# Optimization experiments

Measured on AMD Instinct MI355X. Metric: run time of the kernel, lower is better.

The kernel has to match this reference:

```python
import jax, jax.numpy as jnp
import numpy as np

B, T, C, H = 4, 2048, 1024, 16
HS = C // H  # head_size = 64
FF = 4 * C   # 4096
EPS = 1e-5


def _layernorm(x, g, b):
    mu = jnp.mean(x, axis=-1, keepdims=True)
    var = jnp.mean(jnp.square(x - mu), axis=-1, keepdims=True)
    return (x - mu) * jax.lax.rsqrt(var + EPS) * g + b


def setup_inputs() -> dict:
    key = jax.random.key(0)
    ks = jax.random.split(key, 12)
    s_in = 1.0 / np.sqrt(C)
    s_ff = 1.0 / np.sqrt(FF)
    return {
        "x": jax.random.normal(ks[0], (B, T, C), jnp.float32),
        # per-head projection weights stacked: [H, C, HS]
        "Wq": jax.random.normal(ks[1], (H, C, HS), jnp.float32) * s_in,
        "Wk": jax.random.normal(ks[2], (H, C, HS), jnp.float32) * s_in,
        "Wv": jax.random.normal(ks[3], (H, C, HS), jnp.float32) * s_in,
        "Wo": jax.random.normal(ks[4], (C, C), jnp.float32) * s_in,
        "bo": jnp.zeros((C,), jnp.float32),
        "g1": jnp.ones((C,), jnp.float32),
        "b1": jnp.zeros((C,), jnp.float32),
        "g2": jnp.ones((C,), jnp.float32),
        "b2": jnp.zeros((C,), jnp.float32),
        "W1": jax.random.normal(ks[5], (C, FF), jnp.float32) * s_in,
        "bf1": jnp.zeros((FF,), jnp.float32),
        "W2": jax.random.normal(ks[6], (FF, C), jnp.float32) * s_ff,
        "bf2": jnp.zeros((C,), jnp.float32),
    }


def reference(x, Wq, Wk, Wv, Wo, bo, g1, b1, g2, b2, W1, bf1, W2, bf2):
    # pre-norm
    h = _layernorm(x, g1, b1)                       # [B,T,C]
    q = jnp.einsum('btc,hcd->bhtd', h, Wq)          # [B,H,T,HS]
    k = jnp.einsum('btc,hcd->bhtd', h, Wk)
    v = jnp.einsum('btc,hcd->bhtd', h, Wv)
    w = jnp.einsum('bhtd,bhsd->bhts', q, k) * (HS ** -0.5)  # [B,H,T,S]
    mask = jnp.tril(jnp.ones((T, T), bool))          # causal tril
    w = jnp.where(mask[None, None], w, -jnp.inf)
    # NB: original code softmaxes over dim=1 of [B,T,T], i.e. the QUERY axis
    w = jax.nn.softmax(w, axis=-2)
    o = jnp.einsum('bhts,bhsd->bhtd', w, v)          # [B,H,T,HS]
    o = jnp.transpose(o, (0, 2, 1, 3)).reshape(B, T, C)  # concat heads
    x = x + o @ Wo + bo                              # residual 1 (dropout=0)
    f = _layernorm(x, g2, b2)
    ff = jax.nn.relu(f @ W1 + bf1) @ W2 + bf2        # FFN (dropout=0)
    return x + ff
```

## Files before the change

### kernel.cpp

```cpp
#include <hip/hip_runtime.h>


#define T_SEQ 2048
#define SCALE2 0.1803368801f

typedef __attribute__((ext_vector_type(8))) short short8;
typedef __attribute__((ext_vector_type(4))) float f32x4;

typedef __attribute__((address_space(1))) unsigned int g_u32;
typedef __attribute__((address_space(3))) unsigned int l_u32;

__device__ __forceinline__ unsigned short f2bf(float f) {
  union { float f; unsigned u; } x; x.f = f;
  unsigned r = (x.u + 0x7FFFu + ((x.u >> 16) & 1u)) >> 16;
  return (unsigned short)r;
}
__device__ __forceinline__ float bf2f(unsigned short u) {
  union { unsigned u; float f; } x; x.u = (unsigned)u << 16;
  return x.f;
}

__device__ __forceinline__ void g2lds16(const void* g, void* l) {
  __builtin_amdgcn_global_load_lds((g_u32*)g, (l_u32*)l, 16, 0, 0);
}

__device__ __forceinline__ int xcd_swz(int flat, int nwg) {
  if ((nwg & 7) != 0) return flat;
  return (flat & 7) * (nwg >> 3) + (flat >> 3);
}

template <int EPI, int BN>
__global__ __launch_bounds__(512, 2) void gemm256(
    const unsigned short* __restrict__ A, const unsigned short* __restrict__ Bt,
    int M, int N, int K,
    unsigned short* __restrict__ out16, float* __restrict__ outF,
    const float* __restrict__ bias, const float* __restrict__ resid) {
  constexpr int WN = BN / 4;
  constexpr int FN = WN / 16;
  extern __shared__ unsigned short lds[];
  unsigned short* ldsA = lds;
  unsigned short* ldsB = lds + 2 * 16384;
  const int tid = threadIdx.x, lane = tid & 63, wid = tid >> 6;
  const int wm = wid >> 2, wn = wid & 3;
  const int nx = gridDim.x;
  const int flat = blockIdx.y * nx + blockIdx.x;
  const int swz = xcd_swz(flat, nx * gridDim.y);
  const int mBase = (swz / nx) * 256, nBase = (swz % nx) * BN;

  f32x4 acc[8][FN];
#pragma unroll
  for (int i = 0; i < 8; ++i)
#pragma unroll
    for (int j = 0; j < FN; ++j)
#pragma unroll
      for (int e = 0; e < 4; ++e) acc[i][j][e] = 0.f;

  auto stage = [&](int buf, int kt) {
    const int k0 = kt << 6;
#pragma unroll
    for (int it = 0; it < 4; ++it) {
      int g = it * 512 + tid;
      int row = g >> 3, colL = g & 7;
      int col = colL ^ (row & 7);
      g2lds16(A + ((size_t)(mBase + row) * K + k0 + col * 8),
              &ldsA[buf * 16384 + (it * 512 + wid * 64) * 8]);
    }
#pragma unroll
    for (int it = 0; it < (BN * 8) / 512; ++it) {
      int g = it * 512 + tid;
      int row = g >> 3, colL = g & 7;
      int col = colL ^ (row & 7);
      g2lds16(Bt + ((size_t)(nBase + row) * K + k0 + col * 8),
              &ldsB[buf * (BN * 64) + (it * 512 + wid * 64) * 8]);
    }
  };

  const int nKT = K >> 6;
  stage(0, 0);
  __syncthreads();
  int cur = 0;
  for (int kt = 0; kt < nKT; ++kt) {
    if (kt + 1 < nKT) stage(cur ^ 1, kt + 1);

    short8 bf[FN][2];
#pragma unroll
    for (int fn = 0; fn < FN; ++fn)
#pragma unroll
      for (int ks = 0; ks < 2; ++ks) {
        int r = wn * WN + fn * 16 + (lane & 15);
        int c = (ks * 4 + (lane >> 4)) ^ (r & 7);
        bf[fn][ks] = *(const short8*)&ldsB[cur * (BN * 64) + r * 64 + c * 8];
      }
#pragma unroll
    for (int q = 0; q < 4; ++q) {
      short8 af[2][2];
#pragma unroll
      for (int mf = 0; mf < 2; ++mf)
#pragma unroll
        for (int ks = 0; ks < 2; ++ks) {
          int r = wm * 128 + q * 32 + mf * 16 + (lane & 15);
          int c = (ks * 4 + (lane >> 4)) ^ (r & 7);
          af[mf][ks] = *(const short8*)&ldsA[cur * 16384 + r * 64 + c * 8];
        }
      __builtin_amdgcn_s_setprio(1);
#pragma unroll
      for (int mf = 0; mf < 2; ++mf)
#pragma unroll
        for (int fn = 0; fn < FN; ++fn)
#pragma unroll
          for (int ks = 0; ks < 2; ++ks)
            acc[q * 2 + mf][fn] = __builtin_amdgcn_mfma_f32_16x16x32_bf16(
                af[mf][ks], bf[fn][ks], acc[q * 2 + mf][fn], 0, 0, 0);
      __builtin_amdgcn_s_setprio(0);
    }
    __syncthreads();
    cur ^= 1;
  }

#pragma unroll
  for (int am = 0; am < 8; ++am)
#pragma unroll
    for (int fn = 0; fn < FN; ++fn) {
      int col = nBase + wn * WN + fn * 16 + (lane & 15);
      int row0 = mBase + wm * 128 + am * 16 + ((lane >> 4) << 2);
      if (EPI == 0) {
#pragma unroll
        for (int r = 0; r < 4; ++r)
          out16[(size_t)(row0 + r) * N + col] = f2bf(acc[am][fn][r]);
      } else if (EPI == 1) {
        float bv = bias[col];
#pragma unroll
        for (int r = 0; r < 4; ++r) {
          size_t idx = (size_t)(row0 + r) * N + col;
          outF[idx] = acc[am][fn][r] + bv + resid[idx];
        }
      } else {
        float bv = bias[col];
#pragma unroll
        for (int r = 0; r < 4; ++r)
          out16[(size_t)(row0 + r) * N + col] =
              f2bf(fmaxf(acc[am][fn][r] + bv, 0.f));
      }
    }
}

__global__ __launch_bounds__(256) void ln_bf16(
    const float* __restrict__ x, const float* __restrict__ gw,
    const float* __restrict__ bw, unsigned short* __restrict__ out) {
  __shared__ float red[8];
  const int row = blockIdx.x, tid = threadIdx.x;
  const float4 v = ((const float4*)(x + (size_t)row * 1024))[tid];
  float s = v.x + v.y + v.z + v.w;
  float q = v.x * v.x + v.y * v.y + v.z * v.z + v.w * v.w;
#pragma unroll
  for (int off = 32; off >= 1; off >>= 1) {
    s += __shfl_down(s, off);
    q += __shfl_down(q, off);
  }
  const int lane = tid & 63, wid = tid >> 6;
  if (lane == 0) { red[wid] = s; red[4 + wid] = q; }
  __syncthreads();
  float S = red[0] + red[1] + red[2] + red[3];
  float Q = red[4] + red[5] + red[6] + red[7];
  float mu = S * (1.f / 1024.f);
  float var = Q * (1.f / 1024.f) - mu * mu;
  float rs = rsqrtf(var + 1e-5f);
  int c = tid * 4;
  ushort4 ov;
  ov.x = f2bf((v.x - mu) * rs * gw[c + 0] + bw[c + 0]);
  ov.y = f2bf((v.y - mu) * rs * gw[c + 1] + bw[c + 1]);
  ov.z = f2bf((v.z - mu) * rs * gw[c + 2] + bw[c + 2]);
  ov.w = f2bf((v.w - mu) * rs * gw[c + 3] + bw[c + 3]);
  *(ushort4*)&out[(size_t)row * 1024 + c] = ov;
}

__global__ __launch_bounds__(256) void pack_qkv(
    const float* __restrict__ Wq, const float* __restrict__ Wk,
    const float* __restrict__ Wv, unsigned short* __restrict__ out) {
  __shared__ float tile[64 * 65];
  const int tid = threadIdx.x;
  const float* W = (blockIdx.z == 0) ? Wq : (blockIdx.z == 1) ? Wk : Wv;
  const int h = blockIdx.y, r0 = blockIdx.x * 64;
#pragma unroll
  for (int it = 0; it < 4; ++it) {
    int e4 = it * 256 + tid;
    int r = e4 >> 4, c4 = e4 & 15;
    float4 v = *(const float4*)&W[((size_t)h * 1024 + r0 + r) * 64 + c4 * 4];
    tile[r * 65 + c4 * 4 + 0] = v.x;
    tile[r * 65 + c4 * 4 + 1] = v.y;
    tile[r * 65 + c4 * 4 + 2] = v.z;
    tile[r * 65 + c4 * 4 + 3] = v.w;
  }
  __syncthreads();
#pragma unroll
  for (int it = 0; it < 4; ++it) {
    int e4 = it * 256 + tid;
    int d = e4 >> 4, r4 = e4 & 15;
    ushort4 ov;
    ov.x = f2bf(tile[(r4 * 4 + 0) * 65 + d]);
    ov.y = f2bf(tile[(r4 * 4 + 1) * 65 + d]);
    ov.z = f2bf(tile[(r4 * 4 + 2) * 65 + d]);
    ov.w = f2bf(tile[(r4 * 4 + 3) * 65 + d]);
    *(ushort4*)&out[(size_t)(blockIdx.z * 1024 + h * 64 + d) * 1024 + r0 +
                    r4 * 4] = ov;
  }
}

__global__ __launch_bounds__(256) void transpose_cast(
    const float* __restrict__ in, unsigned short* __restrict__ out, int R,
    int C) {
  __shared__ float tile[64 * 65];
  const int tid = threadIdx.x;
  const int r0 = blockIdx.x * 64, c0 = blockIdx.y * 64;
#pragma unroll
  for (int it = 0; it < 4; ++it) {
    int e4 = it * 256 + tid;
    int r = e4 >> 4, c4 = e4 & 15;
    float4 v = *(const float4*)&in[(size_t)(r0 + r) * C + c0 + c4 * 4];
    tile[r * 65 + c4 * 4 + 0] = v.x;
    tile[r * 65 + c4 * 4 + 1] = v.y;
    tile[r * 65 + c4 * 4 + 2] = v.z;
    tile[r * 65 + c4 * 4 + 3] = v.w;
  }
  __syncthreads();
#pragma unroll
  for (int it = 0; it < 4; ++it) {
    int e4 = it * 256 + tid;
    int c = e4 >> 4, r4 = e4 & 15;
    ushort4 ov;
    ov.x = f2bf(tile[(r4 * 4 + 0) * 65 + c]);
    ov.y = f2bf(tile[(r4 * 4 + 1) * 65 + c]);
    ov.z = f2bf(tile[(r4 * 4 + 2) * 65 + c]);
    ov.w = f2bf(tile[(r4 * 4 + 3) * 65 + c]);
    *(ushort4*)&out[(size_t)(c0 + c) * R + r0 + r4 * 4] = ov;
  }
}

__global__ __launch_bounds__(256) void vtrans(
    const unsigned short* __restrict__ qkv, const float* __restrict__ linv,
    unsigned short* __restrict__ vT) {
  __shared__ unsigned short tile[64 * 66];
  const int tid = threadIdx.x;
  const int bh = blockIdx.y, b = bh >> 4, h = bh & 15;
  const int t0 = blockIdx.x * 64;
#pragma unroll
  for (int it = 0; it < 8; ++it) {
    int e2 = it * 256 + tid;
    int r = e2 >> 5, c2 = e2 & 31;
    unsigned v = *(const unsigned*)&qkv[(size_t)(b * T_SEQ + t0 + r) * 3072 +
                                        2048 + h * 64 + c2 * 2];
    float li = linv[(size_t)bh * T_SEQ + t0 + r];
    unsigned short lo = f2bf(bf2f((unsigned short)(v & 0xffff)) * li);
    unsigned short hi = f2bf(bf2f((unsigned short)(v >> 16)) * li);
    *(unsigned*)&tile[r * 66 + c2 * 2] = (unsigned)lo | ((unsigned)hi << 16);
  }
  __syncthreads();
#pragma unroll
  for (int it = 0; it < 8; ++it) {
    int e2 = it * 256 + tid;
    int d = e2 >> 5, t2 = e2 & 31;
    unsigned short a = tile[(t2 * 2) * 66 + d];
    unsigned short bb = tile[(t2 * 2 + 1) * 66 + d];
    unsigned pk = (unsigned)a | ((unsigned)bb << 16);
    *(unsigned*)&vT[(size_t)(bh * 64 + d) * T_SEQ + t0 + t2 * 2] = pk;
  }
}

__global__ __launch_bounds__(256) void attn_stats(
    const unsigned short* __restrict__ qkv, float* __restrict__ linvOut) {
  __shared__ unsigned short qt[2][64 * 64];
  const int tid = threadIdx.x, lane = tid & 63, w = tid >> 6;
  const int f = xcd_swz(blockIdx.y * 8 + blockIdx.x, 512);
  const int q = f & 7, bh = f >> 3;
  const int b = bh >> 4, h = bh & 15;
  const int sxA = q * 4 + w, sxB = 31 - sxA;
  const int sA = sxA * 64, sB = sxB * 64;
  const int it0 = (q <= 3) ? 4 * q : 28 - 4 * q;

  short8 kfA[4][2], kfB[4][2];
#pragma unroll
  for (int fn = 0; fn < 4; ++fn)
#pragma unroll
    for (int ks = 0; ks < 2; ++ks) {
      int d = 1024 + h * 64 + ks * 32 + ((lane >> 4) << 3);
      kfA[fn][ks] = *(const short8*)&qkv[(size_t)(b * T_SEQ + sA + fn * 16 +
                                                  (lane & 15)) * 3072 + d];
      kfB[fn][ks] = *(const short8*)&qkv[(size_t)(b * T_SEQ + sB + fn * 16 +
                                                  (lane & 15)) * 3072 + d];
    }
  float lA[4] = {0.f, 0.f, 0.f, 0.f}, lB[4] = {0.f, 0.f, 0.f, 0.f};

  auto stageQ = [&](int buf, int ti) {
    int t0 = ti * 64;
#pragma unroll
    for (int it = 0; it < 2; ++it) {
      int g = it * 256 + tid;
      int row = g >> 3;
      int col = (g & 7) ^ (row & 7);
      g2lds16(qkv + ((size_t)(b * T_SEQ + t0 + row) * 3072 + h * 64 + col * 8),
              &qt[buf][(it * 256 + w * 64) * 8]);
    }
  };

  auto accum = [&](const short8 (&af)[2], const short8 (&kf)[4][2],
                   float (&lacc)[4], int sBase, int t0, int mf, bool diag) {
    f32x4 sc[4];
#pragma unroll
    for (int fn = 0; fn < 4; ++fn)
#pragma unroll
      for (int e = 0; e < 4; ++e) sc[fn][e] = 0.f;
    __builtin_amdgcn_s_setprio(1);
#pragma unroll
    for (int fn = 0; fn < 4; ++fn)
#pragma unroll
      for (int ks = 0; ks < 2; ++ks)
        sc[fn] = __builtin_amdgcn_mfma_f32_16x16x32_bf16(af[ks], kf[fn][ks],
                                                         sc[fn], 0, 0, 0);
    __builtin_amdgcn_s_setprio(0);
    const int tRow = t0 + mf * 16 + ((lane >> 4) << 2);
    if (diag) {
#pragma unroll
      for (int fn = 0; fn < 4; ++fn) {
        int s = sBase + fn * 16 + (lane & 15);
#pragma unroll
        for (int r = 0; r < 4; ++r) {
          float e = exp2f(sc[fn][r] * SCALE2);
          lacc[fn] += (tRow + r >= s) ? e : 0.f;
        }
      }
    } else {
#pragma unroll
      for (int fn = 0; fn < 4; ++fn)
#pragma unroll
        for (int r = 0; r < 4; ++r) lacc[fn] += exp2f(sc[fn][r] * SCALE2);
    }
  };

  stageQ(0, it0);
  __syncthreads();
  int cur = 0;
  for (int ti = it0; ti < 32; ++ti) {
    if (ti + 1 < 32) stageQ(cur ^ 1, ti + 1);
    const bool doA = ti >= sxA, doB = ti >= sxB;
    if (doA | doB) {
      const int t0g = ti * 64;
#pragma unroll
      for (int mf = 0; mf < 4; ++mf) {
        short8 af[2];
#pragma unroll
        for (int ks = 0; ks < 2; ++ks) {
          int r = mf * 16 + (lane & 15);
          int c = (ks * 4 + (lane >> 4)) ^ (r & 7);
          af[ks] = *(const short8*)&qt[cur][r * 64 + c * 8];
        }
        if (doA) accum(af, kfA, lA, sA, t0g, mf, ti == sxA);
        if (doB) accum(af, kfB, lB, sB, t0g, mf, ti == sxB);
      }
    }
    __syncthreads();
    cur ^= 1;
  }
#pragma unroll
  for (int fn = 0; fn < 4; ++fn) {
    lA[fn] += __shfl_down(lA[fn], 32);
    lA[fn] += __shfl_down(lA[fn], 16);
    lB[fn] += __shfl_down(lB[fn], 32);
    lB[fn] += __shfl_down(lB[fn], 16);
  }
  if (lane < 16) {
#pragma unroll
    for (int fn = 0; fn < 4; ++fn) {
      linvOut[(size_t)bh * T_SEQ + sA + fn * 16 + lane] = 1.f / lA[fn];
      linvOut[(size_t)bh * T_SEQ + sB + fn * 16 + lane] = 1.f / lB[fn];
    }
  }
}

__global__ __launch_bounds__(256, 2) void attn_pv(
    const unsigned short* __restrict__ qkv, const unsigned short* __restrict__ vT,
    unsigned short* __restrict__ o) {
  __shared__ unsigned short kbuf[2][64 * 64];
  __shared__ unsigned short vbuf[2][64 * 64];
  __shared__ unsigned short pl[256 * 64];
  const int tid = threadIdx.x, lane = tid & 63, wid = tid >> 6;
  const int f = xcd_swz(blockIdx.y * 8 + blockIdx.x, 512);
  const int bx = f & 7, bh = f >> 3;
  const int b = bh >> 4, h = bh & 15;
  const int tA = bx * 128, tB = (15 - bx) * 128;
  const int nSTA = 2 * bx + 2, nSTB = 32 - 2 * bx;

  short8 qfA[2][2], qfB[2][2];
#pragma unroll
  for (int mf = 0; mf < 2; ++mf)
#pragma unroll
    for (int ks = 0; ks < 2; ++ks) {
      int d = h * 64 + ks * 32 + ((lane >> 4) << 3);
      int rloc = wid * 32 + mf * 16 + (lane & 15);
      qfA[mf][ks] =
          *(const short8*)&qkv[(size_t)(b * T_SEQ + tA + rloc) * 3072 + d];
      qfB[mf][ks] =
          *(const short8*)&qkv[(size_t)(b * T_SEQ + tB + rloc) * 3072 + d];
    }
  f32x4 oaccA[2][4], oaccB[2][4];
#pragma unroll
  for (int i = 0; i < 2; ++i)
#pragma unroll
    for (int j = 0; j < 4; ++j)
#pragma unroll
      for (int e = 0; e < 4; ++e) { oaccA[i][j][e] = 0.f; oaccB[i][j][e] = 0.f; }

  auto stage = [&](int buf, int st) {
#pragma unroll
    for (int it = 0; it < 2; ++it) {
      int g = it * 256 + tid;
      int row = g >> 3, colL = g & 7;
      int col = colL ^ (row & 7);
      g2lds16(qkv + ((size_t)(b * T_SEQ + st * 64 + row) * 3072 + 1024 +
                     h * 64 + col * 8),
              &kbuf[buf][(it * 256 + wid * 64) * 8]);
      g2lds16(vT + ((size_t)(bh * 64 + row) * T_SEQ + st * 64 + col * 8),
              &vbuf[buf][(it * 256 + wid * 64) * 8]);
    }
  };

  auto qkstore = [&](const short8 (&qf)[2][2], int rowBase, int tBase, int s0,
                     bool maskNeeded, int cur) {
    f32x4 sc[2][4];
#pragma unroll
    for (int i = 0; i < 2; ++i)
#pragma unroll
      for (int j = 0; j < 4; ++j)
#pragma unroll
        for (int e = 0; e < 4; ++e) sc[i][j][e] = 0.f;
    __builtin_amdgcn_s_setprio(1);
#pragma unroll
    for (int fn = 0; fn < 4; ++fn)
#pragma unroll
      for (int ks = 0; ks < 2; ++ks) {
        int r = fn * 16 + (lane & 15);
        int c = (ks * 4 + (lane >> 4)) ^ (r & 7);
        short8 kfr = *(const short8*)&kbuf[cur][r * 64 + c * 8];
        sc[0][fn] = __builtin_amdgcn_mfma_f32_16x16x32_bf16(qf[0][ks], kfr,
                                                            sc[0][fn], 0, 0, 0);
        sc[1][fn] = __builtin_amdgcn_mfma_f32_16x16x32_bf16(qf[1][ks], kfr,
                                                            sc[1][fn], 0, 0, 0);
      }
    __builtin_amdgcn_s_setprio(0);
#pragma unroll
    for (int fn = 0; fn < 4; ++fn) {
      int sg = s0 + fn * 16 + (lane & 15);
      int colb = (fn * 16 + (lane & 15)) * 2;
#pragma unroll
      for (int mf = 0; mf < 2; ++mf) {
        int rowB = rowBase + wid * 32 + mf * 16 + ((lane >> 4) << 2);
        int tRow = tBase + wid * 32 + mf * 16 + ((lane >> 4) << 2);
#pragma unroll
        for (int r = 0; r < 4; ++r) {
          float p = exp2f(sc[mf][fn][r] * SCALE2);
          if (maskNeeded) p = (tRow + r >= sg) ? p : 0.f;
          int row = rowB + r;
          int byteoff = row * 128 + (colb ^ ((row & 7) << 4));
          *(unsigned short*)((char*)pl + byteoff) = f2bf(p);
        }
      }
    }
  };

  stage(0, 0);
  int cur = 0;
  __syncthreads();

  for (int st = 0; st < nSTB; ++st) {
    const int s0 = st * 64;
    const bool doA = st < nSTA;

    if (doA) qkstore(qfA, 0, tA, s0, st >= nSTA - 2, cur);
    qkstore(qfB, 128, tB, s0, st >= nSTB - 2, cur);
    __syncthreads();

    if (st + 1 < nSTB) stage(cur ^ 1, st + 1);

    __builtin_amdgcn_s_setprio(1);
#pragma unroll
    for (int ks = 0; ks < 2; ++ks) {
      short8 paA[2], paB[2];
#pragma unroll
      for (int mf = 0; mf < 2; ++mf) {
        int rowa = wid * 32 + mf * 16 + (lane & 15);
        int kb = ks * 64 + ((lane >> 4) << 4);
        paB[mf] = *(const short8*)((const char*)pl + (128 + rowa) * 128 +
                                   (kb ^ ((rowa & 7) << 4)));
        if (doA)
          paA[mf] = *(const short8*)((const char*)pl + rowa * 128 +
                                     (kb ^ ((rowa & 7) << 4)));
      }
#pragma unroll
      for (int df = 0; df < 4; ++df) {
        int r = df * 16 + (lane & 15);
        int c = (ks * 4 + (lane >> 4)) ^ (r & 7);
        short8 vb = *(const short8*)&vbuf[cur][r * 64 + c * 8];
        oaccB[0][df] = __builtin_amdgcn_mfma_f32_16x16x32_bf16(paB[0], vb,
                                                               oaccB[0][df], 0, 0, 0);
        oaccB[1][df] = __builtin_amdgcn_mfma_f32_16x16x32_bf16(paB[1], vb,
                                                               oaccB[1][df], 0, 0, 0);
        if (doA) {
          oaccA[0][df] = __builtin_amdgcn_mfma_f32_16x16x32_bf16(paA[0], vb,
                                                                 oaccA[0][df], 0, 0, 0);
          oaccA[1][df] = __builtin_amdgcn_mfma_f32_16x16x32_bf16(paA[1], vb,
                                                                 oaccA[1][df], 0, 0, 0);
        }
      }
    }
    __builtin_amdgcn_s_setprio(0);
    __syncthreads();
    cur ^= 1;
  }
#pragma unroll
  for (int mf = 0; mf < 2; ++mf)
#pragma unroll
    for (int df = 0; df < 4; ++df) {
      int d = h * 64 + df * 16 + (lane & 15);
      int ra = tA + wid * 32 + mf * 16 + ((lane >> 4) << 2);
      int rb = tB + wid * 32 + mf * 16 + ((lane >> 4) << 2);
#pragma unroll
      for (int r = 0; r < 4; ++r) {
        o[(size_t)(b * T_SEQ + ra + r) * 1024 + d] = f2bf(oaccA[mf][df][r]);
        o[(size_t)(b * T_SEQ + rb + r) * 1024 + d] = f2bf(oaccB[mf][df][r]);
      }
    }
}

extern "C" void kernel_launch(void* const* d_in, const int* in_sizes, int n_in,
                              void* d_out, int out_size, void* d_ws,
                              size_t ws_size, hipStream_t stream) {
  const float* x = (const float*)d_in[0];
  const float* Wq = (const float*)d_in[1];
  const float* Wk = (const float*)d_in[2];
  const float* Wv = (const float*)d_in[3];
  const float* Wo = (const float*)d_in[4];
  const float* bo = (const float*)d_in[5];
  const float* g1 = (const float*)d_in[6];
  const float* b1 = (const float*)d_in[7];
  const float* g2 = (const float*)d_in[8];
  const float* b2 = (const float*)d_in[9];
  const float* W1 = (const float*)d_in[10];
  const float* bf1 = (const float*)d_in[11];
  const float* W2 = (const float*)d_in[12];
  const float* bf2 = (const float*)d_in[13];
  float* out = (float*)d_out;

  char* ws = (char*)d_ws;
  size_t off = 0;
  auto alloc = [&](size_t bytes) {
    char* p = ws + off;
    off += (bytes + 255) & ~(size_t)255;
    return p;
  };
  unsigned short* Wqkv = (unsigned short*)alloc(3072ull * 1024 * 2);
  unsigned short* WoT = (unsigned short*)alloc(1024ull * 1024 * 2);
  unsigned short* W1T = (unsigned short*)alloc(4096ull * 1024 * 2);
  unsigned short* W2T = (unsigned short*)alloc(1024ull * 4096 * 2);
  unsigned short* hbuf = (unsigned short*)alloc(8192ull * 1024 * 2);
  char* regionE = alloc(8192ull * 3072 * 2 + 64ull * 64 * 2048 * 2);
  unsigned short* qkv = (unsigned short*)regionE;
  unsigned short* vT = (unsigned short*)(regionE + 8192ull * 3072 * 2);
  unsigned short* act = (unsigned short*)regionE;
  float* lbuf = (float*)alloc(64ull * 2048 * 4);
  float* x1 = (float*)alloc(8192ull * 1024 * 4);
  unsigned short* fbuf = (unsigned short*)alloc(8192ull * 1024 * 2);
  unsigned short* obuf = hbuf;

  (void)in_sizes; (void)n_in; (void)out_size; (void)ws_size;

  const size_t LDS128 = (2 * 16384 + 2 * 128 * 64) * 2;
  const size_t LDS256 = (2 * 16384 + 2 * 256 * 64) * 2;

  pack_qkv<<<dim3(16, 16, 3), 256, 0, stream>>>(Wq, Wk, Wv, Wqkv);
  transpose_cast<<<dim3(16, 16), 256, 0, stream>>>(Wo, WoT, 1024, 1024);
  transpose_cast<<<dim3(16, 64), 256, 0, stream>>>(W1, W1T, 1024, 4096);
  transpose_cast<<<dim3(64, 16), 256, 0, stream>>>(W2, W2T, 4096, 1024);
  ln_bf16<<<8192, 256, 0, stream>>>(x, g1, b1, hbuf);
  gemm256<0, 128><<<dim3(24, 32), 512, LDS128, stream>>>(
      hbuf, Wqkv, 8192, 3072, 1024, qkv, nullptr, nullptr, nullptr);
  attn_stats<<<dim3(8, 64), 256, 0, stream>>>(qkv, lbuf);
  vtrans<<<dim3(32, 64), 256, 0, stream>>>(qkv, lbuf, vT);
  attn_pv<<<dim3(8, 64), 256, 0, stream>>>(qkv, vT, obuf);
  gemm256<1, 128><<<dim3(8, 32), 512, LDS128, stream>>>(
      obuf, WoT, 8192, 1024, 1024, nullptr, x1, bo, x);
  ln_bf16<<<8192, 256, 0, stream>>>(x1, g2, b2, fbuf);
  gemm256<2, 256><<<dim3(16, 32), 512, LDS256, stream>>>(
      fbuf, W1T, 8192, 4096, 1024, act, nullptr, bf1, nullptr);
  gemm256<1, 128><<<dim3(8, 32), 512, LDS128, stream>>>(
      act, W2T, 8192, 1024, 4096, nullptr, out, bf2, x1);
}
```

Before: 477.5 us.

## Split attention column-sum stats across more blocks with per-wave Q staging

The attn_stats kernel is restructured from 512 blocks into 2048 blocks. Each block handles one pair of key tiles and half the query range, and each wave independently streams 32-row Q chunks into its own LDS buffers using explicit vmcnt waits instead of block-wide barriers. Partial column sums are reduced within the block and written as two halves, and vtrans combines them and computes the reciprocal. The aim is more parallelism and occupancy and less barrier stalling, at the cost of redundant K-fragment loads per block and a larger partial-sum buffer. The f2bf helper is also switched to the HIP intrinsic conversion.

```diff
diff --git a/kernel.cpp b/kernel.cpp
--- a/kernel.cpp
+++ b/kernel.cpp
@@ -1,4 +1,5 @@
 #include <hip/hip_runtime.h>
+#include <hip/hip_bf16.h>
 
 
 #define T_SEQ 2048
@@ -11,9 +12,9 @@
 typedef __attribute__((address_space(3))) unsigned int l_u32;
 
 __device__ __forceinline__ unsigned short f2bf(float f) {
-  union { float f; unsigned u; } x; x.f = f;
-  unsigned r = (x.u + 0x7FFFu + ((x.u >> 16) & 1u)) >> 16;
-  return (unsigned short)r;
+  __hip_bfloat16 h = __float2bfloat16(f);
+  union { __hip_bfloat16 h; unsigned short u; } x; x.h = h;
+  return x.u;
 }
 __device__ __forceinline__ float bf2f(unsigned short u) {
   union { unsigned u; float f; } x; x.u = (unsigned)u << 16;
@@ -237,7 +238,7 @@
 }
 
 __global__ __launch_bounds__(256) void vtrans(
-    const unsigned short* __restrict__ qkv, const float* __restrict__ linv,
+    const unsigned short* __restrict__ qkv, const float* __restrict__ lpart,
     unsigned short* __restrict__ vT) {
   __shared__ unsigned short tile[64 * 66];
   const int tid = threadIdx.x;
@@ -249,7 +250,9 @@
     int r = e2 >> 5, c2 = e2 & 31;
     unsigned v = *(const unsigned*)&qkv[(size_t)(b * T_SEQ + t0 + r) * 3072 +
                                         2048 + h * 64 + c2 * 2];
-    float li = linv[(size_t)bh * T_SEQ + t0 + r];
+    float l0 = lpart[(size_t)bh * T_SEQ + t0 + r];
+    float l1 = lpart[(size_t)(64 + bh) * T_SEQ + t0 + r];
+    float li = 1.f / (l0 + l1);
     unsigned short lo = f2bf(bf2f((unsigned short)(v & 0xffff)) * li);
     unsigned short hi = f2bf(bf2f((unsigned short)(v >> 16)) * li);
     *(unsigned*)&tile[r * 66 + c2 * 2] = (unsigned)lo | ((unsigned)hi << 16);
@@ -266,16 +269,17 @@
   }
 }
 
-__global__ __launch_bounds__(256) void attn_stats(
-    const unsigned short* __restrict__ qkv, float* __restrict__ linvOut) {
-  __shared__ unsigned short qt[2][64 * 64];
+__global__ __launch_bounds__(256, 4) void attn_stats(
+    const unsigned short* __restrict__ qkv, float* __restrict__ lpart) {
+  __shared__ unsigned short qt[4][2][32 * 64];
+  __shared__ float redL[4][2][64];
   const int tid = threadIdx.x, lane = tid & 63, w = tid >> 6;
-  const int f = xcd_swz(blockIdx.y * 8 + blockIdx.x, 512);
-  const int q = f & 7, bh = f >> 3;
+  const int f = xcd_swz(blockIdx.y * 32 + blockIdx.x, 2048);
+  const int half = f & 1, px = (f >> 1) & 15, bh = f >> 5;
   const int b = bh >> 4, h = bh & 15;
-  const int sxA = q * 4 + w, sxB = 31 - sxA;
+  const int sxA = px, sxB = 31 - px;
   const int sA = sxA * 64, sB = sxB * 64;
-  const int it0 = (q <= 3) ? 4 * q : 28 - 4 * q;
+  const int m = half * 4 + w;
 
   short8 kfA[4][2], kfB[4][2];
 #pragma unroll
@@ -290,20 +294,20 @@
     }
   float lA[4] = {0.f, 0.f, 0.f, 0.f}, lB[4] = {0.f, 0.f, 0.f, 0.f};
 
-  auto stageQ = [&](int buf, int ti) {
-    int t0 = ti * 64;
-#pragma unroll
-    for (int it = 0; it < 2; ++it) {
-      int g = it * 256 + tid;
+  auto stageQ = [&](int buf, int idx) {
+    int t0 = idx * 32;
+#pragma unroll
+    for (int it = 0; it < 4; ++it) {
+      int g = it * 64 + lane;
       int row = g >> 3;
       int col = (g & 7) ^ (row & 7);
       g2lds16(qkv + ((size_t)(b * T_SEQ + t0 + row) * 3072 + h * 64 + col * 8),
-              &qt[buf][(it * 256 + w * 64) * 8]);
+              &qt[w][buf][it * 512]);
     }
   };
 
   auto accum = [&](const short8 (&af)[2], const short8 (&kf)[4][2],
-                   float (&lacc)[4], int sBase, int t0, int mf, bool diag) {
+                   float (&lacc)[4], int sBase, int tRow, bool diag) {
     f32x4 sc[4];
 #pragma unroll
     for (int fn = 0; fn < 4; ++fn)
@@ -317,48 +321,54 @@
         sc[fn] = __builtin_amdgcn_mfma_f32_16x16x32_bf16(af[ks], kf[fn][ks],
                                                          sc[fn], 0, 0, 0);
     __builtin_amdgcn_s_setprio(0);
-    const int tRow = t0 + mf * 16 + ((lane >> 4) << 2);
     if (diag) {
 #pragma unroll
       for (int fn = 0; fn < 4; ++fn) {
         int s = sBase + fn * 16 + (lane & 15);
-#pragma unroll
-        for (int r = 0; r < 4; ++r) {
-          float e = exp2f(sc[fn][r] * SCALE2);
-          lacc[fn] += (tRow + r >= s) ? e : 0.f;
-        }
+        float e0 = (tRow + 0 >= s) ? exp2f(sc[fn][0] * SCALE2) : 0.f;
+        float e1 = (tRow + 1 >= s) ? exp2f(sc[fn][1] * SCALE2) : 0.f;
+        float e2 = (tRow + 2 >= s) ? exp2f(sc[fn][2] * SCALE2) : 0.f;
+        float e3 = (tRow + 3 >= s) ? exp2f(sc[fn][3] * SCALE2) : 0.f;
+        lacc[fn] += (e0 + e1) + (e2 + e3);
       }
     } else {
 #pragma unroll
-      for (int fn = 0; fn < 4; ++fn)
-#pragma unroll
-        for (int r = 0; r < 4; ++r) lacc[fn] += exp2f(sc[fn][r] * SCALE2);
+      for (int fn = 0; fn < 4; ++fn) {
+        float e0 = exp2f(sc[fn][0] * SCALE2);
+        float e1 = exp2f(sc[fn][1] * SCALE2);
+        float e2 = exp2f(sc[fn][2] * SCALE2);
+        float e3 = exp2f(sc[fn][3] * SCALE2);
+        lacc[fn] += (e0 + e1) + (e2 + e3);
+      }
     }
   };
 
-  stageQ(0, it0);
-  __syncthreads();
+  const int d0 = 2 * sxA - m;
+  const int fi = m + (d0 > 0 ? (((d0 + 7) >> 3) << 3) : 0);
   int cur = 0;
-  for (int ti = it0; ti < 32; ++ti) {
-    if (ti + 1 < 32) stageQ(cur ^ 1, ti + 1);
-    const bool doA = ti >= sxA, doB = ti >= sxB;
-    if (doA | doB) {
-      const int t0g = ti * 64;
-#pragma unroll
-      for (int mf = 0; mf < 4; ++mf) {
-        short8 af[2];
-#pragma unroll
-        for (int ks = 0; ks < 2; ++ks) {
-          int r = mf * 16 + (lane & 15);
-          int c = (ks * 4 + (lane >> 4)) ^ (r & 7);
-          af[ks] = *(const short8*)&qt[cur][r * 64 + c * 8];
-        }
-        if (doA) accum(af, kfA, lA, sA, t0g, mf, ti == sxA);
-        if (doB) accum(af, kfB, lB, sB, t0g, mf, ti == sxB);
-      }
-    }
-    __syncthreads();
-    cur ^= 1;
+  if (fi < 64) stageQ(0, fi);
+  for (int idx = fi; idx < 64; idx += 8, cur ^= 1) {
+    if (idx + 8 < 64) {
+      stageQ(cur ^ 1, idx + 8);
+      asm volatile("s_waitcnt vmcnt(4)" ::: "memory");
+    } else {
+      asm volatile("s_waitcnt vmcnt(0)" ::: "memory");
+    }
+    const int t0g = idx * 32;
+    const bool doB = idx >= 2 * sxB;
+#pragma unroll
+    for (int mf = 0; mf < 2; ++mf) {
+      short8 af[2];
+#pragma unroll
+      for (int ks = 0; ks < 2; ++ks) {
+        int r = mf * 16 + (lane & 15);
+        int c = (ks * 4 + (lane >> 4)) ^ (r & 7);
+        af[ks] = *(const short8*)&qt[w][cur][r * 64 + c * 8];
+      }
+      int tRow = t0g + mf * 16 + ((lane >> 4) << 2);
+      accum(af, kfA, lA, sA, tRow, idx <= 2 * sxA + 1);
+      if (doB) accum(af, kfB, lB, sB, tRow, idx <= 2 * sxB + 1);
+    }
   }
 #pragma unroll
   for (int fn = 0; fn < 4; ++fn) {
@@ -370,9 +380,17 @@
   if (lane < 16) {
 #pragma unroll
     for (int fn = 0; fn < 4; ++fn) {
-      linvOut[(size_t)bh * T_SEQ + sA + fn * 16 + lane] = 1.f / lA[fn];
-      linvOut[(size_t)bh * T_SEQ + sB + fn * 16 + lane] = 1.f / lB[fn];
-    }
+      redL[w][0][fn * 16 + lane] = lA[fn];
+      redL[w][1][fn * 16 + lane] = lB[fn];
+    }
+  }
+  __syncthreads();
+  if (tid < 128) {
+    int which = tid >> 6;
+    float l = redL[0][which][lane] + redL[1][which][lane] +
+              redL[2][which][lane] + redL[3][which][lane];
+    int sbase = (which == 0) ? sA : sB;
+    lpart[((size_t)half * 64 + bh) * T_SEQ + sbase + lane] = l;
   }
 }
 
@@ -565,7 +583,7 @@
   unsigned short* qkv = (unsigned short*)regionE;
   unsigned short* vT = (unsigned short*)(regionE + 8192ull * 3072 * 2);
   unsigned short* act = (unsigned short*)regionE;
-  float* lbuf = (float*)alloc(64ull * 2048 * 4);
+  float* lbuf = (float*)alloc(128ull * 2048 * 4);
   float* x1 = (float*)alloc(8192ull * 1024 * 4);
   unsigned short* fbuf = (unsigned short*)alloc(8192ull * 1024 * 2);
   unsigned short* obuf = hbuf;
@@ -582,7 +600,7 @@
   ln_bf16<<<8192, 256, 0, stream>>>(x, g1, b1, hbuf);
   gemm256<0, 128><<<dim3(24, 32), 512, LDS128, stream>>>(
       hbuf, Wqkv, 8192, 3072, 1024, qkv, nullptr, nullptr, nullptr);
-  attn_stats<<<dim3(8, 64), 256, 0, stream>>>(qkv, lbuf);
+  attn_stats<<<dim3(32, 64), 256, 0, stream>>>(qkv, lbuf);
   vtrans<<<dim3(32, 64), 256, 0, stream>>>(qkv, lbuf, vT);
   attn_pv<<<dim3(8, 64), 256, 0, stream>>>(qkv, vT, obuf);
   gemm256<1, 128><<<dim3(8, 32), 512, LDS128, stream>>>(
```

Result: faster. 437.6 us (-8.4%).
